# Kernel tuning notes

Measured on AMD Instinct MI355X. Metric: run time of the kernel, lower is better.

The kernel has to match this reference:

```python
import jax, jax.numpy as jnp
import numpy as np

B, T, D, H = 8, 1024, 1024, 16
HD = D // H  # 64
FF = 4 * D


def setup_inputs() -> dict:
    key = jax.random.key(0)
    ks = jax.random.split(key, 16)
    s = lambda k, shape, scale: (jax.random.normal(k, shape, dtype=jnp.float32) * scale)
    return {
        "x": s(ks[0], (B, T, D), 1.0),
        "ln1_g": jnp.ones((D,), jnp.float32),
        "ln1_b": jnp.zeros((D,), jnp.float32),
        "ln2_g": jnp.ones((D,), jnp.float32),
        "ln2_b": jnp.zeros((D,), jnp.float32),
        "Wq": s(ks[1], (H, D, HD), 0.02), "bq": jnp.zeros((H, HD), jnp.float32),
        "Wk": s(ks[2], (H, D, HD), 0.02), "bk": jnp.zeros((H, HD), jnp.float32),
        "Wv": s(ks[3], (H, D, HD), 0.02), "bv": jnp.zeros((H, HD), jnp.float32),
        "Wo": s(ks[4], (D, D), 0.02), "bo": jnp.zeros((D,), jnp.float32),
        "W1": s(ks[5], (D, FF), 0.02), "b1": jnp.zeros((FF,), jnp.float32),
        "W2": s(ks[6], (FF, D), 0.02), "b2": jnp.zeros((D,), jnp.float32),
    }


def layer_norm(x, g, b, eps=1e-5):
    mu = jnp.mean(x, axis=-1, keepdims=True)
    var = jnp.mean(jnp.square(x - mu), axis=-1, keepdims=True)
    return (x - mu) * jax.lax.rsqrt(var + eps) * g + b


def reference(x, ln1_g, ln1_b, ln2_g, ln2_b, Wq, bq, Wk, bk, Wv, bv, Wo, bo, W1, b1, W2, b2):
    h = layer_norm(x, ln1_g, ln1_b)
    # Per-head Q/K/V projections, batched over heads (equivalent to the
    # Python loop of per-head Linears in the original module).
    q = jnp.einsum("btd,hde->bhte", h, Wq) + bq[None, :, None, :]
    k = jnp.einsum("btd,hde->bhte", h, Wk) + bk[None, :, None, :]
    v = jnp.einsum("btd,hde->bhte", h, Wv) + bv[None, :, None, :]
    scores = jnp.einsum("bhte,bhse->bhts", q, k) / jnp.sqrt(jnp.float32(HD))
    att = jax.nn.softmax(scores, axis=-1)  # no causal mask in source
    ctx = jnp.einsum("bhts,bhse->bhte", att, v)
    # concat heads along feature dim
    ctx = jnp.transpose(ctx, (0, 2, 1, 3)).reshape(B, T, D)
    attn_out = ctx @ Wo + bo
    x = x + attn_out
    h2 = layer_norm(x, ln2_g, ln2_b)
    ff = jax.nn.gelu(h2 @ W1 + b1, approximate=False) @ W2 + b2
    return x + ff
```

## Files before the change

### kernel.cpp

```cpp
#include <hip/hip_runtime.h>
#include <hip/hip_bf16.h>
#include <cstdint>
#include <cstddef>


typedef __bf16 bf16;
typedef __bf16 bf16x8 __attribute__((ext_vector_type(8)));
typedef __bf16 bf16x4 __attribute__((ext_vector_type(4)));
typedef float  f32x4  __attribute__((ext_vector_type(4)));
typedef uint32_t u32x4 __attribute__((ext_vector_type(4)));

#define BB    8
#define TT    1024
#define DD    1024
#define HH    16
#define HDIM  64
#define FFD   4096
#define MROWS (BB*TT)

__device__ __forceinline__ void async_ld16(const void* g, void* l) {
  __builtin_amdgcn_global_load_lds(
      (const __attribute__((address_space(1))) uint32_t*)g,
      (__attribute__((address_space(3))) uint32_t*)l, 16, 0, 0);
}

__device__ __forceinline__ float gelu_f(float v) {
  float z = 0.7978845608028654f * (v + 0.044715f * v * v * v);
  z = fminf(fmaxf(z, -9.0f), 9.0f);
  const float e = __expf(-2.0f * z);
  const float th = 1.0f - __fdividef(2.0f * e, 1.0f + e);
  return 0.5f * v * (1.0f + th);
}

__device__ __forceinline__ float exp2_fast(float x) {
  float r; asm("v_exp_f32 %0, %1" : "=v"(r) : "v"(x)); return r;
}
__device__ __forceinline__ uint32_t cvt_pk_bf16(float a, float b) {
  uint32_t r; asm("v_cvt_pk_bf16_f32 %0, %1, %2" : "=v"(r) : "v"(a), "v"(b));
  return r;
}

__global__ void k_transpose_cast(const float* __restrict__ src, bf16* __restrict__ dst,
                                 int K, int N) {
  __shared__ float tile[32][33];
  const size_t boff = (size_t)blockIdx.z * K * N;
  src += boff; dst += boff;
  const int k0 = blockIdx.y * 32, n0 = blockIdx.x * 32;
  const int tx = threadIdx.x, ty = threadIdx.y;
#pragma unroll
  for (int i = 0; i < 4; ++i)
    tile[ty + i*8][tx] = src[(size_t)(k0 + ty + i*8) * N + n0 + tx];
  __syncthreads();
#pragma unroll
  for (int i = 0; i < 4; ++i)
    dst[(size_t)(n0 + ty + i*8) * K + k0 + tx] = (bf16)tile[tx][ty + i*8];
}

__global__ void k_concat_bias(const float* __restrict__ bq, const float* __restrict__ bk,
                              const float* __restrict__ bv, float* __restrict__ out) {
  int i = blockIdx.x * 256 + threadIdx.x;
  float v = (i < 1024) ? bq[i] : (i < 2048) ? bk[i - 1024] : bv[i - 2048];
  out[i] = v;
}

__global__ void k_transpose_v(const bf16* __restrict__ qkv, bf16* __restrict__ vT) {
  __shared__ bf16 tile[32][33];
  const int bh = blockIdx.z;
  const int b = bh >> 4, h = bh & 15;
  const int t0 = blockIdx.x * 32, e0 = blockIdx.y * 32;
  const int tx = threadIdx.x, ty = threadIdx.y;
  const bf16* src = qkv + (size_t)b * TT * 3072 + 2048 + h * 64;
#pragma unroll
  for (int i = 0; i < 4; ++i)
    tile[ty + i*8][tx] = src[(size_t)(t0 + ty + i*8) * 3072 + e0 + tx];
  __syncthreads();
  bf16* dst = vT + ((size_t)bh * 64 + e0) * TT + t0;
#pragma unroll
  for (int i = 0; i < 4; ++i)
    dst[(size_t)(ty + i*8) * TT + tx] = tile[tx][ty + i*8];
}

__global__ void k_layernorm(const float* __restrict__ x, const float* __restrict__ g,
                            const float* __restrict__ b, bf16* __restrict__ out) {
  const int row = blockIdx.x, tid = threadIdx.x;
  const float* xr = x + (size_t)row * DD;
  f32x4 v = *(const f32x4*)(xr + tid * 4);
  float s  = v[0] + v[1] + v[2] + v[3];
  float ss = v[0]*v[0] + v[1]*v[1] + v[2]*v[2] + v[3]*v[3];
#pragma unroll
  for (int m = 1; m < 64; m <<= 1) { s += __shfl_xor(s, m); ss += __shfl_xor(ss, m); }
  __shared__ float red[8];
  const int wid = tid >> 6;
  if ((tid & 63) == 0) { red[wid*2] = s; red[wid*2+1] = ss; }
  __syncthreads();
  s  = red[0] + red[2] + red[4] + red[6];
  ss = red[1] + red[3] + red[5] + red[7];
  const float mu = s * (1.0f / DD);
  const float var = ss * (1.0f / DD) - mu * mu;
  const float rs = rsqrtf(var + 1e-5f);
  bf16x4 o;
#pragma unroll
  for (int j = 0; j < 4; ++j)
    o[j] = (bf16)((v[j] - mu) * rs * g[tid*4 + j] + b[tid*4 + j]);
  *(bf16x4*)&out[(size_t)row * DD + tid * 4] = o;
}

template<int MODE>
__global__ __launch_bounds__(512, 2)
void k_gemm256(const bf16* __restrict__ A, const bf16* __restrict__ Bt,
               const float* __restrict__ bias, bf16* __restrict__ outb,
               int M, int N, int K) {
  __shared__ __align__(16) bf16 As[2][256 * 64];
  __shared__ __align__(16) bf16 Bs[2][256 * 64];
  const int tid = threadIdx.x;
  const int w = tid >> 6, l = tid & 63;
  const int wm = w >> 2, wn = w & 3;
  const int l15 = l & 15, l4 = l >> 4;

  const int nbx = N >> 8;
  const int nwg = gridDim.x;
  const int cpx = nwg >> 3;
  const int swz = (blockIdx.x & 7) * cpx + (blockIdx.x >> 3);
  const int m0 = (swz / nbx) << 8, n0 = (swz % nbx) << 8;

  f32x4 acc[8][4] = {};

  const int l7 = l15 & 7;
  const int c0 = (l4 ^ l7) * 8;
  const int c1 = ((4 + l4) ^ l7) * 8;
  const bf16* const A00 = &As[0][(wm*128 + l15)*64 + c0];
  const bf16* const A01 = &As[0][(wm*128 + l15)*64 + c1];
  const bf16* const A10 = &As[1][(wm*128 + l15)*64 + c0];
  const bf16* const A11 = &As[1][(wm*128 + l15)*64 + c1];
  const bf16* const B00 = &Bs[0][(wn*64 + l15)*64 + c0];
  const bf16* const B01 = &Bs[0][(wn*64 + l15)*64 + c1];
  const bf16* const B10 = &Bs[1][(wn*64 + l15)*64 + c0];
  const bf16* const B11 = &Bs[1][(wn*64 + l15)*64 + c1];

  const int srow = l >> 3, sch = l & 7;
  const int schx = (sch ^ srow) * 8;
  const bf16* const aG0 = A  + (size_t)(m0 + w*8 + srow) * K + schx;
  const bf16* const aG1 = aG0 + (size_t)64 * K;
  const bf16* const aG2 = aG0 + (size_t)128 * K;
  const bf16* const aG3 = aG0 + (size_t)192 * K;
  const bf16* const bG0 = Bt + (size_t)(n0 + w*8 + srow) * K + schx;
  const bf16* const bG1 = bG0 + (size_t)64 * K;
  const bf16* const bG2 = bG0 + (size_t)128 * K;
  const bf16* const bG3 = bG0 + (size_t)192 * K;
  bf16* const LA0 = (bf16*)As[0] + w*512;
  bf16* const LA1 = (bf16*)As[1] + w*512;
  bf16* const LB0 = (bf16*)Bs[0] + w*512;
  bf16* const LB1 = (bf16*)Bs[1] + w*512;

  const int NT = K >> 6;

#define RD_B(reg, base) { _Pragma("unroll") \
    for (int nf = 0; nf < 4; ++nf) reg[nf] = *(const bf16x8*)((base) + nf*1024); }
#define RD_A(reg, base, mb) { _Pragma("unroll") \
    for (int mf = 0; mf < 4; ++mf) reg[mf] = *(const bf16x8*)((base) + (mb+mf)*1024); }
#define MM(areg, breg, mb) { _Pragma("unroll") \
    for (int mf = 0; mf < 4; ++mf) _Pragma("unroll") \
      for (int nf = 0; nf < 4; ++nf) \
        acc[mb+mf][nf] = __builtin_amdgcn_mfma_f32_16x16x32_bf16(areg[mf], breg[nf], acc[mb+mf][nf], 0, 0, 0); }
#define SGA(off, lb) { async_ld16(aG0 + (off), (lb)+0*64);  async_ld16(aG1 + (off), (lb)+64*64); \
                       async_ld16(aG2 + (off), (lb)+128*64); async_ld16(aG3 + (off), (lb)+192*64); }
#define SGB2a(off, lb) { async_ld16(bG0 + (off), (lb)+0*64);   async_ld16(bG1 + (off), (lb)+64*64); }
#define SGB2b(off, lb) { async_ld16(bG2 + (off), (lb)+128*64); async_ld16(bG3 + (off), (lb)+192*64); }
#define WAIT_LGKM { asm volatile("s_waitcnt lgkmcnt(0)" ::: "memory"); __builtin_amdgcn_sched_barrier(0); }
#define BAR __builtin_amdgcn_s_barrier()

  SGA(0, LA0)  SGB2a(0, LB0) SGB2b(0, LB0)  SGA(64, LA1)
  asm volatile("s_waitcnt vmcnt(4)" ::: "memory");
  __builtin_amdgcn_sched_barrier(0);
  BAR;

  size_t ko = 0;
  for (int T = 0; T < NT; T += 2) {
    const bool nl  = (T + 2 < NT);
    const bool nl2 = (T + 3 < NT);
    bf16x8 b0[4], b1[4], alo[4], ahi[4];

    RD_B(b0, B00) RD_A(alo, A00, 0)
    SGB2a(ko + 64, LB1)
    BAR; WAIT_LGKM;
    __builtin_amdgcn_s_setprio(1); MM(alo, b0, 0) __builtin_amdgcn_s_setprio(0);
    BAR;
    RD_A(ahi, A00, 4)
    SGB2b(ko + 64, LB1)
    BAR; WAIT_LGKM;
    __builtin_amdgcn_s_setprio(1); MM(ahi, b0, 4) __builtin_amdgcn_s_setprio(0);
    BAR;
    RD_B(b1, B01) RD_A(alo, A01, 0) RD_A(ahi, A01, 4)
    BAR; WAIT_LGKM;
    __builtin_amdgcn_s_setprio(1); MM(alo, b1, 0) __builtin_amdgcn_s_setprio(0);
    BAR;
    if (nl) SGA(ko + 128, LA0)
    __builtin_amdgcn_s_setprio(1); MM(ahi, b1, 4) __builtin_amdgcn_s_setprio(0);
    if (nl) { asm volatile("s_waitcnt vmcnt(4)" ::: "memory"); }
    else    { asm volatile("s_waitcnt vmcnt(0)" ::: "memory"); }
    __builtin_amdgcn_sched_barrier(0);
    BAR;

    RD_B(b0, B10) RD_A(alo, A10, 0)
    if (nl) SGB2a(ko + 128, LB0)
    BAR; WAIT_LGKM;
    __builtin_amdgcn_s_setprio(1); MM(alo, b0, 0) __builtin_amdgcn_s_setprio(0);
    BAR;
    RD_A(ahi, A10, 4)
    if (nl) SGB2b(ko + 128, LB0)
    BAR; WAIT_LGKM;
    __builtin_amdgcn_s_setprio(1); MM(ahi, b0, 4) __builtin_amdgcn_s_setprio(0);
    BAR;
    RD_B(b1, B11) RD_A(alo, A11, 0) RD_A(ahi, A11, 4)
    BAR; WAIT_LGKM;
    __builtin_amdgcn_s_setprio(1); MM(alo, b1, 0) __builtin_amdgcn_s_setprio(0);
    BAR;
    if (nl2) SGA(ko + 192, LA1)
    __builtin_amdgcn_s_setprio(1); MM(ahi, b1, 4) __builtin_amdgcn_s_setprio(0);
    if (nl2) { asm volatile("s_waitcnt vmcnt(4)" ::: "memory"); }
    else     { asm volatile("s_waitcnt vmcnt(0)" ::: "memory"); }
    __builtin_amdgcn_sched_barrier(0);
    BAR;

    ko += 128;
  }
#undef RD_B
#undef RD_A
#undef MM
#undef SGA
#undef SGB2a
#undef SGB2b
#undef WAIT_LGKM
#undef BAR

#pragma unroll
  for (int mf = 0; mf < 8; ++mf) {
#pragma unroll
    for (int r = 0; r < 4; ++r) {
      const size_t grow = (size_t)(m0 + wm*128 + mf*16 + l4*4 + r);
      const size_t rowoff = grow * (size_t)N;
#pragma unroll
      for (int nf = 0; nf < 4; ++nf) {
        const int gcol = n0 + wn*64 + nf*16 + l15;
        float v = acc[mf][nf][r] + bias[gcol];
        if constexpr (MODE == 1) v = gelu_f(v);
        outb[rowoff + gcol] = (bf16)v;
      }
    }
  }
}

template<int MODE>
__global__ __launch_bounds__(256)
void k_gemm(const bf16* __restrict__ A, const bf16* __restrict__ Bt,
            const float* __restrict__ bias, const float* __restrict__ res,
            bf16* __restrict__ outb, float* __restrict__ outf,
            int M, int N, int K) {
  __shared__ __align__(16) bf16 As[128 * 64];
  __shared__ __align__(16) bf16 Bs[128 * 64];
  const int tid = threadIdx.x;
  const int w = tid >> 6, l = tid & 63;
  const int wm = w >> 1, wn = w & 1;
  const int l15 = l & 15, l4 = l >> 4;
  const int m0 = blockIdx.y * 128, n0 = blockIdx.x * 128;

  f32x4 acc[4][4] = {};

  const int l7 = l15 & 7;
  const int c0 = (l4 ^ l7) * 8, c1 = ((4 + l4) ^ l7) * 8;
  const bf16* const Ab = &As[(wm*64 + l15)*64];
  const bf16* const Bb = &Bs[(wn*64 + l15)*64];

  const int sr8 = l >> 3, sl7 = l & 7;
  const int schx = (sl7 ^ sr8) * 8;
  const bf16* const gA0 = A  + (size_t)(m0 + w*32 + sr8) * K + schx;
  const bf16* const gA1 = gA0 + (size_t)8 * K;
  const bf16* const gA2 = gA0 + (size_t)16 * K;
  const bf16* const gA3 = gA0 + (size_t)24 * K;
  const bf16* const gB0 = Bt + (size_t)(n0 + w*32 + sr8) * K + schx;
  const bf16* const gB1 = gB0 + (size_t)8 * K;
  const bf16* const gB2 = gB0 + (size_t)16 * K;
  const bf16* const gB3 = gB0 + (size_t)24 * K;
  bf16* const lA = (bf16*)As + w*32*64;
  bf16* const lB = (bf16*)Bs + w*32*64;

  for (int k0 = 0; k0 < K; k0 += 64) {
    async_ld16(gA0 + k0, lA);          async_ld16(gA1 + k0, lA + 8*64);
    async_ld16(gA2 + k0, lA + 16*64);  async_ld16(gA3 + k0, lA + 24*64);
    async_ld16(gB0 + k0, lB);          async_ld16(gB1 + k0, lB + 8*64);
    async_ld16(gB2 + k0, lB + 16*64);  async_ld16(gB3 + k0, lB + 24*64);
    __syncthreads();
#pragma unroll
    for (int kk = 0; kk < 2; ++kk) {
      const int cc = kk ? c1 : c0;
      bf16x8 af[4], bfr[4];
#pragma unroll
      for (int mf = 0; mf < 4; ++mf) af[mf] = *(const bf16x8*)(Ab + mf*1024 + cc);
#pragma unroll
      for (int nf = 0; nf < 4; ++nf) bfr[nf] = *(const bf16x8*)(Bb + nf*1024 + cc);
#pragma unroll
      for (int mf = 0; mf < 4; ++mf)
#pragma unroll
        for (int nf = 0; nf < 4; ++nf)
          acc[mf][nf] = __builtin_amdgcn_mfma_f32_16x16x32_bf16(af[mf], bfr[nf], acc[mf][nf], 0, 0, 0);
    }
    __syncthreads();
  }

#pragma unroll
  for (int mf = 0; mf < 4; ++mf) {
#pragma unroll
    for (int r = 0; r < 4; ++r) {
      const size_t grow = (size_t)(m0 + wm*64 + mf*16 + l4*4 + r);
      const size_t rowoff = grow * (size_t)N;
#pragma unroll
      for (int nf = 0; nf < 4; ++nf) {
        const int gcol = n0 + wn*64 + nf*16 + l15;
        float v = acc[mf][nf][r] + bias[gcol];
        if constexpr (MODE == 1) v = gelu_f(v);
        if constexpr (MODE == 2) {
          v += res[rowoff + gcol];
          outf[rowoff + gcol] = v;
        } else {
          outb[rowoff + gcol] = (bf16)v;
        }
      }
    }
  }
}

__global__ __launch_bounds__(512)
void k_attn(const bf16* __restrict__ qkv, const bf16* __restrict__ vT,
            bf16* __restrict__ ctx) {
  const int tid = threadIdx.x;
  const int w = tid >> 6, l = tid & 63;
  const int l15 = l & 15, l4 = l >> 4;

  const int gid = ((int)blockIdx.x & 7) * 128 + ((int)blockIdx.x >> 3);
  const int qt = gid & 7;
  const int bh = gid >> 3;
  const int h = bh & 15, b = bh >> 4;

  __shared__ __align__(16) bf16 Ks[2][64 * 64];
  __shared__ __align__(16) bf16 Vs[2][64 * 64];

  const bf16* base = qkv + (size_t)b * TT * 3072;
  const bf16* Qp = base + h * 64;
  const bf16* Kp = base + 1024 + h * 64;
  const bf16* Vtp = vT + (size_t)bh * HDIM * TT;

  const float SCL = 0.125f * 1.44269504f;
  const float THR = 8.0f * 1.44269504f;

  const int qrow = qt * 128 + w * 16 + l15;
  bf16x8 qf[2];
  {
    bf16x8 q0 = *(const bf16x8*)&Qp[(size_t)qrow * 3072 + l4 * 8];
    bf16x8 q1 = *(const bf16x8*)&Qp[(size_t)qrow * 3072 + 32 + l4 * 8];
#pragma unroll
    for (int j = 0; j < 8; ++j) {
      qf[0][j] = (bf16)((float)q0[j] * SCL);
      qf[1][j] = (bf16)((float)q1[j] * SCL);
    }
  }

  f32x4 oacc[4] = {};
  float mrow = -1e30f;
  float lrow = 0.f;

  const int l7 = l15 & 7;
  const int c0 = (l4 ^ l7) * 8, c1 = ((4 + l4) ^ l7) * 8;

  const int aL0 = (((l4 & 1) << 5) + l15) << 2;
  const int aL1 = aL0 + 64;
  const bool hi = (l & 32) != 0;

  const int srow = w * 8 + (l >> 3);
  const int sch = (l & 7) ^ (srow & 7);

  auto stage = [&](int buf, int t) {
    const int kv0 = t * 64;
    async_ld16(Kp + (size_t)(kv0 + srow) * 3072 + sch * 8, &Ks[buf][w * 512]);
    async_ld16(Vtp + (size_t)srow * TT + kv0 + sch * 8, &Vs[buf][w * 512]);
  };

  stage(0, 0);
  for (int t = 0; t < TT / 64; ++t) {
    const int cur = t & 1;
    __syncthreads();
    if (t + 1 < TT / 64) stage(cur ^ 1, t + 1);

    const bf16* const Kc = &Ks[cur][l15 * 64];
    const bf16* const Vc = &Vs[cur][l15 * 64];

    f32x4 sacc[4] = {};
    __builtin_amdgcn_s_setprio(1);
#pragma unroll
    for (int nf = 0; nf < 4; ++nf) {
      bf16x8 k0 = *(const bf16x8*)(Kc + nf*1024 + c0);
      bf16x8 k1 = *(const bf16x8*)(Kc + nf*1024 + c1);
      sacc[nf] = __builtin_amdgcn_mfma_f32_16x16x32_bf16(k0, qf[0], sacc[nf], 0, 0, 0);
      sacc[nf] = __builtin_amdgcn_mfma_f32_16x16x32_bf16(k1, qf[1], sacc[nf], 0, 0, 0);
    }
    __builtin_amdgcn_s_setprio(0);

    float m = fmaxf(fmaxf(sacc[0][0], sacc[0][1]), fmaxf(sacc[0][2], sacc[0][3]));
#pragma unroll
    for (int nf = 1; nf < 4; ++nf)
      m = fmaxf(m, fmaxf(fmaxf(sacc[nf][0], sacc[nf][1]), fmaxf(sacc[nf][2], sacc[nf][3])));
    m = fmaxf(m, __shfl_xor(m, 16));
    m = fmaxf(m, __shfl_xor(m, 32));

    const int ok = (m <= mrow + THR);
    if (!__all(ok)) {
      const float mn = fmaxf(mrow, m);
      const float e = exp2_fast(mrow - mn);
      mrow = mn;
      lrow *= e;
      const int qb = l4 << 2;
      float e0 = __shfl(e, qb + 0), e1 = __shfl(e, qb + 1);
      float e2 = __shfl(e, qb + 2), e3 = __shfl(e, qb + 3);
#pragma unroll
      for (int nf = 0; nf < 4; ++nf) {
        oacc[nf][0] *= e0; oacc[nf][1] *= e1;
        oacc[nf][2] *= e2; oacc[nf][3] *= e3;
      }
    }

    float p[4][4];
    float ls = 0.f;
    uint32_t pk0[4], pk1[4];
#pragma unroll
    for (int nf = 0; nf < 4; ++nf) {
#pragma unroll
      for (int r = 0; r < 4; ++r) {
        p[nf][r] = exp2_fast(sacc[nf][r] - mrow);
        ls += p[nf][r];
      }
      pk0[nf] = cvt_pk_bf16(p[nf][0], p[nf][1]);
      pk1[nf] = cvt_pk_bf16(p[nf][2], p[nf][3]);
    }
    ls += __shfl_xor(ls, 16);
    ls += __shfl_xor(ls, 32);
    lrow += ls;

    __builtin_amdgcn_s_setprio(1);
#pragma unroll
    for (int kk = 0; kk < 2; ++kk) {
      const int nfa = 2*kk, nfb = 2*kk + 1;
      int u0 = __builtin_amdgcn_ds_bpermute(aL0, (int)pk0[nfa]);
      int u1 = __builtin_amdgcn_ds_bpermute(aL0, (int)pk0[nfb]);
      int v0 = __builtin_amdgcn_ds_bpermute(aL0, (int)pk1[nfa]);
      int v1 = __builtin_amdgcn_ds_bpermute(aL0, (int)pk1[nfb]);
      int x0 = __builtin_amdgcn_ds_bpermute(aL1, (int)pk0[nfa]);
      int x1 = __builtin_amdgcn_ds_bpermute(aL1, (int)pk0[nfb]);
      int y0 = __builtin_amdgcn_ds_bpermute(aL1, (int)pk1[nfa]);
      int y1 = __builtin_amdgcn_ds_bpermute(aL1, (int)pk1[nfb]);
      u32x4 pw;
      pw[0] = (uint32_t)(hi ? u1 : u0);
      pw[1] = (uint32_t)(hi ? v1 : v0);
      pw[2] = (uint32_t)(hi ? x1 : x0);
      pw[3] = (uint32_t)(hi ? y1 : y0);
      bf16x8 pa = __builtin_bit_cast(bf16x8, pw);
      const int cc = kk ? c1 : c0;
#pragma unroll
      for (int nf = 0; nf < 4; ++nf) {
        bf16x8 vb = *(const bf16x8*)(Vc + nf*1024 + cc);
        oacc[nf] = __builtin_amdgcn_mfma_f32_16x16x32_bf16(pa, vb, oacc[nf], 0, 0, 0);
      }
    }
    __builtin_amdgcn_s_setprio(0);
  }

  const int qb = l4 << 2;
  float li0 = 1.0f / __shfl(lrow, qb + 0);
  float li1 = 1.0f / __shfl(lrow, qb + 1);
  float li2 = 1.0f / __shfl(lrow, qb + 2);
  float li3 = 1.0f / __shfl(lrow, qb + 3);
  bf16* outp = ctx + ((size_t)b * TT + qt * 128 + w * 16) * DD + h * 64;
#pragma unroll
  for (int nf = 0; nf < 4; ++nf) {
    outp[(size_t)(qb + 0) * DD + l15 + nf*16] = (bf16)(oacc[nf][0] * li0);
    outp[(size_t)(qb + 1) * DD + l15 + nf*16] = (bf16)(oacc[nf][1] * li1);
    outp[(size_t)(qb + 2) * DD + l15 + nf*16] = (bf16)(oacc[nf][2] * li2);
    outp[(size_t)(qb + 3) * DD + l15 + nf*16] = (bf16)(oacc[nf][3] * li3);
  }
}

extern "C" void kernel_launch(void* const* d_in, const int* in_sizes, int n_in,
                              void* d_out, int out_size, void* d_ws, size_t ws_size,
                              hipStream_t stream) {
  const float* x     = (const float*)d_in[0];
  const float* ln1_g = (const float*)d_in[1];
  const float* ln1_b = (const float*)d_in[2];
  const float* ln2_g = (const float*)d_in[3];
  const float* ln2_b = (const float*)d_in[4];
  const float* Wq    = (const float*)d_in[5];
  const float* bq    = (const float*)d_in[6];
  const float* Wk    = (const float*)d_in[7];
  const float* bk    = (const float*)d_in[8];
  const float* Wv    = (const float*)d_in[9];
  const float* bv    = (const float*)d_in[10];
  const float* Wo    = (const float*)d_in[11];
  const float* bo    = (const float*)d_in[12];
  const float* W1    = (const float*)d_in[13];
  const float* b1    = (const float*)d_in[14];
  const float* W2    = (const float*)d_in[15];
  const float* b2    = (const float*)d_in[16];
  float* out = (float*)d_out;

  char* ws = (char*)d_ws;
  bf16* h1    = (bf16*)(ws + 0);
  bf16* vT    = (bf16*)(ws + 0);
  bf16* qkv   = (bf16*)(ws + 16777216);
  bf16* ctx   = (bf16*)(ws + 67108864);
  bf16* u     = (bf16*)(ws + 16777216);
  float* x1   = (float*)(ws + 83886080);
  bf16* wtqkv = (bf16*)(ws + 117440512);
  bf16* wot   = (bf16*)(ws + 123731968);
  bf16* w1t   = (bf16*)(ws + 125829120);
  bf16* w2t   = (bf16*)(ws + 134217728);
  float* bqkv = (float*)(ws + 142606336);
  bf16* h2 = h1;

  dim3 tb(32, 8);
  k_transpose_cast<<<dim3(2, 32, 16), tb, 0, stream>>>(Wq, wtqkv, DD, HDIM);
  k_transpose_cast<<<dim3(2, 32, 16), tb, 0, stream>>>(Wk, wtqkv + 1024*1024, DD, HDIM);
  k_transpose_cast<<<dim3(2, 32, 16), tb, 0, stream>>>(Wv, wtqkv + 2048*1024, DD, HDIM);
  k_transpose_cast<<<dim3(32, 32, 1), tb, 0, stream>>>(Wo, wot, DD, DD);
  k_transpose_cast<<<dim3(128, 32, 1), tb, 0, stream>>>(W1, w1t, DD, FFD);
  k_transpose_cast<<<dim3(32, 128, 1), tb, 0, stream>>>(W2, w2t, FFD, DD);
  k_concat_bias<<<dim3(12), 256, 0, stream>>>(bq, bk, bv, bqkv);

  k_layernorm<<<dim3(MROWS), 256, 0, stream>>>(x, ln1_g, ln1_b, h1);

  k_gemm256<0><<<dim3((MROWS/256)*(3072/256)), 512, 0, stream>>>(
      h1, wtqkv, bqkv, qkv, MROWS, 3072, DD);

  k_transpose_v<<<dim3(32, 2, 128), tb, 0, stream>>>(qkv, vT);

  k_attn<<<dim3(1024), 512, 0, stream>>>(qkv, vT, ctx);

  k_gemm<2><<<dim3(8, 64), 256, 0, stream>>>(ctx, wot, bo, x,
                                             nullptr, x1, MROWS, DD, DD);

  k_layernorm<<<dim3(MROWS), 256, 0, stream>>>(x1, ln2_g, ln2_b, h2);

  k_gemm256<1><<<dim3((MROWS/256)*(FFD/256)), 512, 0, stream>>>(
      h2, w1t, b1, u, MROWS, FFD, DD);

  k_gemm<2><<<dim3(8, 64), 256, 0, stream>>>(u, w2t, b2, x1,
                                             nullptr, out, MROWS, DD, FFD);

  (void)in_sizes; (void)n_in; (void)out_size; (void)ws_size;
}
```

Measured before the change: 416.5 us.

## Add 256x128 GEMM for QKV projection and re-pipeline FFN1 GEMM prefetch

Adds a new GEMM kernel with 256x128 output tiles for the QKV projection, giving 768 workgroups instead of 384 so the grid fills the CUs more evenly. The FFN1 GEMM gets a restructured pipeline: A and B tile loads are split into finer quarter/half pieces spread across eight MFMA phases, waiting at vmcnt(2). A fragments are read in halves so fewer registers stay live. The smaller tile reloads A more often per output and does less MFMA work per barrier. The finer prefetch schedule adds more synchronisation points.

```diff
diff --git a/kernel.cpp b/kernel.cpp
--- a/kernel.cpp
+++ b/kernel.cpp
@@ -105,26 +105,143 @@
   *(bf16x4*)&out[(size_t)row * DD + tid * 4] = o;
 }
 
+#define RD_B(reg, base) { _Pragma("unroll") \
+    for (int nf = 0; nf < 4; ++nf) reg[nf] = *(const bf16x8*)((base) + nf*1024); }
+#define RD_A4(reg, base, mb) { _Pragma("unroll") \
+    for (int mf = 0; mf < 4; ++mf) reg[mf] = *(const bf16x8*)((base) + (mb+mf)*1024); }
+#define MM(areg, breg, mb) { _Pragma("unroll") \
+    for (int mf = 0; mf < 4; ++mf) _Pragma("unroll") \
+      for (int nf = 0; nf < 4; ++nf) \
+        acc[mb+mf][nf] = __builtin_amdgcn_mfma_f32_16x16x32_bf16(areg[mf], breg[nf], acc[mb+mf][nf], 0, 0, 0); }
+#define SGA(off, lb) { async_ld16(aG0 + (off), (lb)+0*64);   async_ld16(aG1 + (off), (lb)+64*64); \
+                       async_ld16(aG2 + (off), (lb)+128*64); async_ld16(aG3 + (off), (lb)+192*64); }
+#define SGA_S0(off, lb) { async_ld16(aG0 + (off), (lb)+0*64);    async_ld16(aG2 + (off), (lb)+128*64); }
+#define SGA_S1(off, lb) { async_ld16(aG1 + (off), (lb)+64*64);   async_ld16(aG3 + (off), (lb)+192*64); }
+#define SGB_Q0(off, lb) { async_ld16(bG0 + (off), (lb)+0*64);    async_ld16(bG1 + (off), (lb)+64*64); }
+#define SGB_Q1(off, lb) { async_ld16(bG2 + (off), (lb)+128*64);  async_ld16(bG3 + (off), (lb)+192*64); }
+#define WAIT_LGKM { asm volatile("s_waitcnt lgkmcnt(0)" ::: "memory"); __builtin_amdgcn_sched_barrier(0); }
+#define VMC(n)  { asm volatile("s_waitcnt vmcnt(" #n ")" ::: "memory"); __builtin_amdgcn_sched_barrier(0); }
+#define BAR __builtin_amdgcn_s_barrier()
+#define PR1 __builtin_amdgcn_s_setprio(1)
+#define PR0 __builtin_amdgcn_s_setprio(0)
+
 template<int MODE>
 __global__ __launch_bounds__(512, 2)
-void k_gemm256(const bf16* __restrict__ A, const bf16* __restrict__ Bt,
-               const float* __restrict__ bias, bf16* __restrict__ outb,
-               int M, int N, int K) {
+void k_gemm256n(const bf16* __restrict__ A, const bf16* __restrict__ Bt,
+                const float* __restrict__ bias, bf16* __restrict__ outb,
+                int M, int N, int K) {
+  __shared__ __align__(16) bf16 As[2][256 * 64];
+  __shared__ __align__(16) bf16 Bs[2][128 * 64];
+  const int tid = threadIdx.x;
+  const int w = tid >> 6, l = tid & 63;
+  const int wm = w >> 1, wn = w & 1;
+  const int l15 = l & 15, l4 = l >> 4;
+  const int nbx = N >> 7;
+  const int nwg = gridDim.x;
+  const int cpx = nwg >> 3;
+  const int swz = (blockIdx.x & 7) * cpx + (blockIdx.x >> 3);
+  const int m0 = (swz / nbx) << 8, n0 = (swz % nbx) << 7;
+  f32x4 acc[4][4] = {};
+  const int l7 = l15 & 7;
+  const int c0 = (l4 ^ l7) * 8;
+  const int c1 = ((4 + l4) ^ l7) * 8;
+  const bf16* const A00 = &As[0][(wm*64 + l15)*64 + c0];
+  const bf16* const A01 = &As[0][(wm*64 + l15)*64 + c1];
+  const bf16* const A10 = &As[1][(wm*64 + l15)*64 + c0];
+  const bf16* const A11 = &As[1][(wm*64 + l15)*64 + c1];
+  const bf16* const B00 = &Bs[0][(wn*64 + l15)*64 + c0];
+  const bf16* const B01 = &Bs[0][(wn*64 + l15)*64 + c1];
+  const bf16* const B10 = &Bs[1][(wn*64 + l15)*64 + c0];
+  const bf16* const B11 = &Bs[1][(wn*64 + l15)*64 + c1];
+  const int srow = l >> 3, sch = l & 7;
+  const int schx = (sch ^ srow) * 8;
+  const bf16* const aG0 = A  + (size_t)(m0 + w*8 + srow) * K + schx;
+  const bf16* const aG1 = aG0 + (size_t)64 * K;
+  const bf16* const aG2 = aG0 + (size_t)128 * K;
+  const bf16* const aG3 = aG0 + (size_t)192 * K;
+  const bf16* const bG0 = Bt + (size_t)(n0 + w*8 + srow) * K + schx;
+  const bf16* const bG1 = bG0 + (size_t)64 * K;
+  bf16* const LA0 = (bf16*)As[0] + w*512;
+  bf16* const LA1 = (bf16*)As[1] + w*512;
+  bf16* const LB0 = (bf16*)Bs[0] + w*512;
+  bf16* const LB1 = (bf16*)Bs[1] + w*512;
+  const int NT = K >> 6;
+
+#define SGB2(off, lb) { async_ld16(bG0 + (off), (lb)+0*64); async_ld16(bG1 + (off), (lb)+64*64); }
+
+  SGA(0, LA0)  SGB2(0, LB0)
+  SGA(64, LA1) SGB2(64, LB1)
+  VMC(6);
+  BAR;
+
+  size_t ko = 0;
+  for (int T = 0; T < NT; T += 2) {
+    const bool nl  = (T + 2 < NT);
+    const bool nl2 = (T + 3 < NT);
+    bf16x8 b0[4], b1[4], a[4], a2[4];
+
+    RD_B(b0, B00) RD_A4(a, A00, 0)
+    BAR; WAIT_LGKM;
+    PR1; MM(a, b0, 0) PR0;
+    BAR;
+    RD_B(b1, B01) RD_A4(a2, A01, 0)
+    BAR; WAIT_LGKM;
+    PR1; MM(a2, b1, 0) PR0;
+    BAR;
+    if (nl) { SGA(ko + 128, LA0) SGB2(ko + 128, LB0) }
+    if (nl) { VMC(6); } else { VMC(0); }
+    BAR;
+
+    RD_B(b0, B10) RD_A4(a, A10, 0)
+    BAR; WAIT_LGKM;
+    PR1; MM(a, b0, 0) PR0;
+    BAR;
+    RD_B(b1, B11) RD_A4(a2, A11, 0)
+    BAR; WAIT_LGKM;
+    PR1; MM(a2, b1, 0) PR0;
+    BAR;
+    if (nl2) { SGA(ko + 192, LA1) SGB2(ko + 192, LB1) }
+    if (nl2) { VMC(6); } else { VMC(0); }
+    BAR;
+
+    ko += 128;
+  }
+#undef SGB2
+
+#pragma unroll
+  for (int mf = 0; mf < 4; ++mf) {
+#pragma unroll
+    for (int r = 0; r < 4; ++r) {
+      const size_t grow = (size_t)(m0 + wm*64 + mf*16 + l4*4 + r);
+      const size_t rowoff = grow * (size_t)N;
+#pragma unroll
+      for (int nf = 0; nf < 4; ++nf) {
+        const int gcol = n0 + wn*64 + nf*16 + l15;
+        float v = acc[mf][nf][r] + bias[gcol];
+        if constexpr (MODE == 1) v = gelu_f(v);
+        outb[rowoff + gcol] = (bf16)v;
+      }
+    }
+  }
+}
+
+template<int MODE>
+__global__ __launch_bounds__(512, 2)
+void k_gemm256p(const bf16* __restrict__ A, const bf16* __restrict__ Bt,
+                const float* __restrict__ bias, bf16* __restrict__ outb,
+                int M, int N, int K) {
   __shared__ __align__(16) bf16 As[2][256 * 64];
   __shared__ __align__(16) bf16 Bs[2][256 * 64];
   const int tid = threadIdx.x;
   const int w = tid >> 6, l = tid & 63;
   const int wm = w >> 2, wn = w & 3;
   const int l15 = l & 15, l4 = l >> 4;
-
   const int nbx = N >> 8;
   const int nwg = gridDim.x;
   const int cpx = nwg >> 3;
   const int swz = (blockIdx.x & 7) * cpx + (blockIdx.x >> 3);
   const int m0 = (swz / nbx) << 8, n0 = (swz % nbx) << 8;
-
   f32x4 acc[8][4] = {};
-
   const int l7 = l15 & 7;
   const int c0 = (l4 ^ l7) * 8;
   const int c1 = ((4 + l4) ^ l7) * 8;
@@ -136,7 +253,6 @@
   const bf16* const B01 = &Bs[0][(wn*64 + l15)*64 + c1];
   const bf16* const B10 = &Bs[1][(wn*64 + l15)*64 + c0];
   const bf16* const B11 = &Bs[1][(wn*64 + l15)*64 + c1];
-
   const int srow = l >> 3, sch = l & 7;
   const int schx = (sch ^ srow) * 8;
   const bf16* const aG0 = A  + (size_t)(m0 + w*8 + srow) * K + schx;
@@ -151,87 +267,66 @@
   bf16* const LA1 = (bf16*)As[1] + w*512;
   bf16* const LB0 = (bf16*)Bs[0] + w*512;
   bf16* const LB1 = (bf16*)Bs[1] + w*512;
-
   const int NT = K >> 6;
 
-#define RD_B(reg, base) { _Pragma("unroll") \
-    for (int nf = 0; nf < 4; ++nf) reg[nf] = *(const bf16x8*)((base) + nf*1024); }
-#define RD_A(reg, base, mb) { _Pragma("unroll") \
-    for (int mf = 0; mf < 4; ++mf) reg[mf] = *(const bf16x8*)((base) + (mb+mf)*1024); }
-#define MM(areg, breg, mb) { _Pragma("unroll") \
-    for (int mf = 0; mf < 4; ++mf) _Pragma("unroll") \
-      for (int nf = 0; nf < 4; ++nf) \
-        acc[mb+mf][nf] = __builtin_amdgcn_mfma_f32_16x16x32_bf16(areg[mf], breg[nf], acc[mb+mf][nf], 0, 0, 0); }
-#define SGA(off, lb) { async_ld16(aG0 + (off), (lb)+0*64);  async_ld16(aG1 + (off), (lb)+64*64); \
-                       async_ld16(aG2 + (off), (lb)+128*64); async_ld16(aG3 + (off), (lb)+192*64); }
-#define SGB2a(off, lb) { async_ld16(bG0 + (off), (lb)+0*64);   async_ld16(bG1 + (off), (lb)+64*64); }
-#define SGB2b(off, lb) { async_ld16(bG2 + (off), (lb)+128*64); async_ld16(bG3 + (off), (lb)+192*64); }
-#define WAIT_LGKM { asm volatile("s_waitcnt lgkmcnt(0)" ::: "memory"); __builtin_amdgcn_sched_barrier(0); }
-#define BAR __builtin_amdgcn_s_barrier()
-
-  SGA(0, LA0)  SGB2a(0, LB0) SGB2b(0, LB0)  SGA(64, LA1)
-  asm volatile("s_waitcnt vmcnt(4)" ::: "memory");
-  __builtin_amdgcn_sched_barrier(0);
+  SGA_S0(0, LA0) SGA_S1(0, LA0)
+  SGB_Q0(0, LB0) SGB_Q1(0, LB0)
+  SGA_S0(64, LA1)
+  VMC(2);
   BAR;
 
   size_t ko = 0;
   for (int T = 0; T < NT; T += 2) {
-    const bool nl  = (T + 2 < NT);
-    const bool nl2 = (T + 3 < NT);
-    bf16x8 b0[4], b1[4], alo[4], ahi[4];
-
-    RD_B(b0, B00) RD_A(alo, A00, 0)
-    SGB2a(ko + 64, LB1)
-    BAR; WAIT_LGKM;
-    __builtin_amdgcn_s_setprio(1); MM(alo, b0, 0) __builtin_amdgcn_s_setprio(0);
-    BAR;
-    RD_A(ahi, A00, 4)
-    SGB2b(ko + 64, LB1)
-    BAR; WAIT_LGKM;
-    __builtin_amdgcn_s_setprio(1); MM(ahi, b0, 4) __builtin_amdgcn_s_setprio(0);
-    BAR;
-    RD_B(b1, B01) RD_A(alo, A01, 0) RD_A(ahi, A01, 4)
-    BAR; WAIT_LGKM;
-    __builtin_amdgcn_s_setprio(1); MM(alo, b1, 0) __builtin_amdgcn_s_setprio(0);
-    BAR;
-    if (nl) SGA(ko + 128, LA0)
-    __builtin_amdgcn_s_setprio(1); MM(ahi, b1, 4) __builtin_amdgcn_s_setprio(0);
-    if (nl) { asm volatile("s_waitcnt vmcnt(4)" ::: "memory"); }
-    else    { asm volatile("s_waitcnt vmcnt(0)" ::: "memory"); }
-    __builtin_amdgcn_sched_barrier(0);
-    BAR;
-
-    RD_B(b0, B10) RD_A(alo, A10, 0)
-    if (nl) SGB2a(ko + 128, LB0)
-    BAR; WAIT_LGKM;
-    __builtin_amdgcn_s_setprio(1); MM(alo, b0, 0) __builtin_amdgcn_s_setprio(0);
-    BAR;
-    RD_A(ahi, A10, 4)
-    if (nl) SGB2b(ko + 128, LB0)
-    BAR; WAIT_LGKM;
-    __builtin_amdgcn_s_setprio(1); MM(ahi, b0, 4) __builtin_amdgcn_s_setprio(0);
-    BAR;
-    RD_B(b1, B11) RD_A(alo, A11, 0) RD_A(ahi, A11, 4)
-    BAR; WAIT_LGKM;
-    __builtin_amdgcn_s_setprio(1); MM(alo, b1, 0) __builtin_amdgcn_s_setprio(0);
-    BAR;
-    if (nl2) SGA(ko + 192, LA1)
-    __builtin_amdgcn_s_setprio(1); MM(ahi, b1, 4) __builtin_amdgcn_s_setprio(0);
-    if (nl2) { asm volatile("s_waitcnt vmcnt(4)" ::: "memory"); }
-    else     { asm volatile("s_waitcnt vmcnt(0)" ::: "memory"); }
-    __builtin_amdgcn_sched_barrier(0);
+    const bool s2 = (T + 2 < NT);
+    const bool s3 = (T + 3 < NT);
+    bf16x8 b0[4], b1[4], a[4];
+
+    RD_B(b0, B00) RD_A4(a, A00, 0)
+    SGA_S1(ko + 64, LA1)
+    BAR; WAIT_LGKM;
+    PR1; MM(a, b0, 0) PR0;
+    BAR;
+    RD_B(b1, B01) RD_A4(a, A01, 0)
+    SGB_Q0(ko + 64, LB1)
+    BAR; WAIT_LGKM;
+    PR1; MM(a, b1, 0) PR0;
+    BAR;
+    RD_A4(a, A00, 4)
+    SGB_Q1(ko + 64, LB1)
+    BAR; WAIT_LGKM;
+    PR1; MM(a, b0, 4) PR0;
+    BAR;
+    RD_A4(a, A01, 4)
+    if (s2) SGA_S0(ko + 128, LA0)
+    BAR; WAIT_LGKM;
+    PR1; MM(a, b1, 4) PR0;
+    if (s2) { VMC(2); } else { VMC(0); }
+    BAR;
+
+    RD_B(b0, B10) RD_A4(a, A10, 0)
+    if (s2) SGA_S1(ko + 128, LA0)
+    BAR; WAIT_LGKM;
+    PR1; MM(a, b0, 0) PR0;
+    BAR;
+    RD_B(b1, B11) RD_A4(a, A11, 0)
+    if (s2) SGB_Q0(ko + 128, LB0)
+    BAR; WAIT_LGKM;
+    PR1; MM(a, b1, 0) PR0;
+    BAR;
+    RD_A4(a, A10, 4)
+    if (s2) SGB_Q1(ko + 128, LB0)
+    BAR; WAIT_LGKM;
+    PR1; MM(a, b0, 4) PR0;
+    BAR;
+    RD_A4(a, A11, 4)
+    if (s3) SGA_S0(ko + 192, LA1)
+    BAR; WAIT_LGKM;
+    PR1; MM(a, b1, 4) PR0;
+    if (s3) { VMC(2); } else { VMC(0); }
     BAR;
 
     ko += 128;
   }
-#undef RD_B
-#undef RD_A
-#undef MM
-#undef SGA
-#undef SGB2a
-#undef SGB2b
-#undef WAIT_LGKM
-#undef BAR
 
 #pragma unroll
   for (int mf = 0; mf < 8; ++mf) {
@@ -534,7 +629,7 @@
 
   k_layernorm<<<dim3(MROWS), 256, 0, stream>>>(x, ln1_g, ln1_b, h1);
 
-  k_gemm256<0><<<dim3((MROWS/256)*(3072/256)), 512, 0, stream>>>(
+  k_gemm256n<0><<<dim3((MROWS/256)*(3072/128)), 512, 0, stream>>>(
       h1, wtqkv, bqkv, qkv, MROWS, 3072, DD);
 
   k_transpose_v<<<dim3(32, 2, 128), tb, 0, stream>>>(qkv, vT);
@@ -546,7 +641,7 @@
 
   k_layernorm<<<dim3(MROWS), 256, 0, stream>>>(x1, ln2_g, ln2_b, h2);
 
-  k_gemm256<1><<<dim3((MROWS/256)*(FFD/256)), 512, 0, stream>>>(
+  k_gemm256p<1><<<dim3((MROWS/256)*(FFD/256)), 512, 0, stream>>>(
       h2, w1t, b1, u, MROWS, FFD, DD);
 
   k_gemm<2><<<dim3(8, 64), 256, 0, stream>>>(u, w2t, b2, x1,
```

Result: no change. 414.6 us (-0.4%).
